# Optimization experiments

Measured on AMD Instinct MI355X. Metric: run time of the kernel, lower is better.

Reference implementation:

```python
import jax, jax.numpy as jnp
import numpy as np

EPS = 1e-5

def _ln(x, g, b):
    mu = jnp.mean(x, axis=-1, keepdims=True)
    var = jnp.mean(jnp.square(x - mu), axis=-1, keepdims=True)
    return (x - mu) * jax.lax.rsqrt(var + EPS) * g + b

def _gelu_new(x):
    # GPT-2 'gelu_new' (tanh approximation)
    c = jnp.asarray(np.sqrt(2.0 / np.pi), x.dtype)
    return 0.5 * x * (1.0 + jnp.tanh(c * (x + 0.044715 * x * x * x)))

def setup_inputs() -> dict:
    key = jax.random.key(0)
    ks = jax.random.split(key, 8)
    B, H, NH, HD, S = 16, 2048, 16, 128, 4096
    inv = lambda n: 1.0 / np.sqrt(n)
    return {
        "hidden_states": jax.random.normal(ks[0], (B, 1, H), jnp.float32),
        "cached_k": jax.random.normal(ks[1], (B, NH, S, HD), jnp.float32),
        "cached_v": jax.random.normal(ks[2], (B, NH, S, HD), jnp.float32),
        "ln1_g": jnp.ones((H,), jnp.float32),
        "ln1_b": jnp.zeros((H,), jnp.float32),
        "W_qkv": jax.random.normal(ks[3], (H, 3 * H), jnp.float32) * inv(H),
        "b_qkv": jnp.zeros((3 * H,), jnp.float32),
        "W_proj": jax.random.normal(ks[4], (H, H), jnp.float32) * inv(H),
        "b_proj": jnp.zeros((H,), jnp.float32),
        "ln2_g": jnp.ones((H,), jnp.float32),
        "ln2_b": jnp.zeros((H,), jnp.float32),
        "W_fc": jax.random.normal(ks[5], (H, 4 * H), jnp.float32) * inv(H),
        "b_fc": jnp.zeros((4 * H,), jnp.float32),
        "W_out": jax.random.normal(ks[6], (4 * H, H), jnp.float32) * inv(4 * H),
        "b_out": jnp.zeros((H,), jnp.float32),
    }

def reference(hidden_states, cached_k, cached_v, ln1_g, ln1_b, W_qkv, b_qkv,
              W_proj, b_proj, ln2_g, ln2_b, W_fc, b_fc, W_out, b_out):
    B, T, H = hidden_states.shape  # T == 1 (decode step)
    NH, HD = cached_k.shape[1], cached_k.shape[3]
    residual = hidden_states
    x = _ln(hidden_states, ln1_g, ln1_b)
    qkv = x @ W_qkv + b_qkv                        # [B,1,3H]
    q, k, v = jnp.split(qkv, 3, axis=-1)
    split = lambda t: t.reshape(B, T, NH, HD).transpose(0, 2, 1, 3)  # [B,NH,T,HD]
    q, k, v = split(q), split(k), split(v)
    k_full = jnp.concatenate([cached_k, k], axis=2)  # [B,NH,S+1,HD]
    v_full = jnp.concatenate([cached_v, v], axis=2)
    scale = 1.0 / jnp.sqrt(jnp.asarray(HD, q.dtype))
    scores = jnp.einsum('bhqd,bhkd->bhqk', q, k_full) * scale
    probs = jax.nn.softmax(scores, axis=-1)
    attn = jnp.einsum('bhqk,bhkd->bhqd', probs, v_full)  # [B,NH,1,HD]
    attn = attn.transpose(0, 2, 1, 3).reshape(B, T, H)
    attn = attn @ W_proj + b_proj
    h = attn + residual
    residual = h
    y = _ln(h, ln2_g, ln2_b)
    y = _gelu_new(y @ W_fc + b_fc) @ W_out + b_out
    return residual + y
```

## Files before the change

kernel.cpp:

```cpp
#include <hip/hip_runtime.h>
#include <hip/hip_bf16.h>

typedef unsigned int uint;


__global__ __launch_bounds__(256) void ln_f32_kernel(const float* __restrict__ in,
    const float* __restrict__ g, const float* __restrict__ bb, float* __restrict__ out)
{
    int row = blockIdx.x, t = threadIdx.x;
    const float* rp = in + row*2048;
    float4 a = ((const float4*)rp)[2*t];
    float4 b = ((const float4*)rp)[2*t+1];
    float v[8] = {a.x,a.y,a.z,a.w,b.x,b.y,b.z,b.w};
    float s=0.f, s2=0.f;
    #pragma unroll
    for(int i=0;i<8;i++){ s+=v[i]; s2+=v[i]*v[i]; }
    #pragma unroll
    for(int o=32;o>0;o>>=1){ s += __shfl_xor(s,o); s2 += __shfl_xor(s2,o); }
    __shared__ float red[8];
    int wv=t>>6, ln=t&63;
    if(ln==0){ red[wv]=s; red[4+wv]=s2; }
    __syncthreads();
    s  = red[0]+red[1]+red[2]+red[3];
    s2 = red[4]+red[5]+red[6]+red[7];
    float mu = s*(1.f/2048.f);
    float var = s2*(1.f/2048.f) - mu*mu;
    float rs = rsqrtf(var + 1e-5f);
    float4 g0 = ((const float4*)g)[2*t],  g1 = ((const float4*)g)[2*t+1];
    float4 b0 = ((const float4*)bb)[2*t], b1 = ((const float4*)bb)[2*t+1];
    float* op = out + row*2048 + t*8;
    float4 o0 = make_float4((v[0]-mu)*rs*g0.x+b0.x, (v[1]-mu)*rs*g0.y+b0.y,
                            (v[2]-mu)*rs*g0.z+b0.z, (v[3]-mu)*rs*g0.w+b0.w);
    float4 o1 = make_float4((v[4]-mu)*rs*g1.x+b1.x, (v[5]-mu)*rs*g1.y+b1.y,
                            (v[6]-mu)*rs*g1.z+b1.z, (v[7]-mu)*rs*g1.w+b1.w);
    ((float4*)op)[0]=o0; ((float4*)op)[1]=o1;
}

template<int KCHUNK>
__global__ __launch_bounds__(256) void gemm_sk(const float* __restrict__ X,
    const float* __restrict__ W, float* __restrict__ part, int K, int N, int colchunks)
{
    __shared__ float XS[16][KCHUNK];
    int cc = blockIdx.x % colchunks;
    int kc = blockIdx.x / colchunks;
    int k0 = kc * KCHUNK;
    for (int idx = threadIdx.x; idx < 16*KCHUNK; idx += 256){
        int m = idx / KCHUNK, i = idx % KCHUNK;
        XS[m][i] = X[m*K + k0 + i];
    }
    __syncthreads();
    int n0 = cc*512 + threadIdx.x*2;
    float a0[16], a1[16];
    #pragma unroll
    for(int m=0;m<16;m++){ a0[m]=0.f; a1[m]=0.f; }
    const float* Wp = W + (size_t)k0*N + n0;
    for (int i=0;i<KCHUNK;i+=4){
        float2 w0 = *(const float2*)(Wp + (size_t)(i+0)*N);
        float2 w1 = *(const float2*)(Wp + (size_t)(i+1)*N);
        float2 w2 = *(const float2*)(Wp + (size_t)(i+2)*N);
        float2 w3 = *(const float2*)(Wp + (size_t)(i+3)*N);
        #pragma unroll
        for(int m=0;m<16;m++){
            float4 x4 = *(const float4*)&XS[m][i];
            a0[m] += x4.x*w0.x + x4.y*w1.x + x4.z*w2.x + x4.w*w3.x;
            a1[m] += x4.x*w0.y + x4.y*w1.y + x4.z*w2.y + x4.w*w3.y;
        }
    }
    #pragma unroll
    for(int m=0;m<16;m++){
        *(float2*)&part[((size_t)(kc*16+m))*N + n0] = make_float2(a0[m], a1[m]);
    }
}

__global__ __launch_bounds__(256) void reduce_sk(const float* __restrict__ part, int N, int splitk,
    const float* __restrict__ bias, const float* __restrict__ res,
    float* __restrict__ outf, int mode)
{
    int n = blockIdx.x*256 + threadIdx.x;
    int m = blockIdx.y;
    size_t stride = (size_t)16*N;
    const float* p = part + (size_t)m*N + n;
    float s = 0.f;
    for (int kc=0;kc<splitk;kc++) s += p[(size_t)kc*stride];
    s += bias[n];
    if (mode==1 || mode==3) s += res[m*N+n];
    if (mode==2){
        float x = s;
        float t = tanhf(0.7978845608028654f*(x + 0.044715f*x*x*x));
        s = 0.5f*x*(1.f+t);
    }
    outf[m*N+n] = s;
}

__global__ __launch_bounds__(256) void attn_chunk(const float* __restrict__ qkv,
    const float* __restrict__ Kc, const float* __restrict__ Vc, float* __restrict__ part)
{
    int h = blockIdx.y, b = blockIdx.z;
    int wave = threadIdx.x >> 6, lane = threadIdx.x & 63;
    int wc = blockIdx.x*4 + wave;
    int jstart = wc * 128;
    const float* qrow = qkv + b*6144 + h*128;
    float2 q = *(const float2*)(qrow + 2*lane);
    size_t bh = (size_t)(b*16+h);
    const float* kp = Kc + bh*4096*128 + (size_t)jstart*128 + 2*lane;
    const float* vp = Vc + bh*4096*128 + (size_t)jstart*128 + 2*lane;
    float m = -1e30f, l = 0.f, o0 = 0.f, o1 = 0.f;
    #pragma unroll 4
    for (int j=0;j<128;++j){
        float2 kw = *(const float2*)kp;
        float2 vw = *(const float2*)vp;
        kp += 128; vp += 128;
        float p = q.x*kw.x + q.y*kw.y;
        p += __shfl_xor(p,32); p += __shfl_xor(p,16); p += __shfl_xor(p,8);
        p += __shfl_xor(p,4);  p += __shfl_xor(p,2);  p += __shfl_xor(p,1);
        float sc = p * 0.08838834764831845f;
        float mn = fmaxf(m, sc);
        float f  = __expf(m - mn);
        float e  = __expf(sc - mn);
        l  = l*f + e;
        o0 = o0*f + e*vw.x;
        o1 = o1*f + e*vw.y;
        m = mn;
    }
    if (wc == 31){
        const float* kn = qkv + b*6144 + 2048 + h*128;
        const float* vn = qkv + b*6144 + 4096 + h*128;
        float p = q.x*kn[2*lane] + q.y*kn[2*lane+1];
        p += __shfl_xor(p,32); p += __shfl_xor(p,16); p += __shfl_xor(p,8);
        p += __shfl_xor(p,4);  p += __shfl_xor(p,2);  p += __shfl_xor(p,1);
        float sc = p * 0.08838834764831845f;
        float mn = fmaxf(m, sc);
        float f  = __expf(m - mn);
        float e  = __expf(sc - mn);
        l  = l*f + e;
        o0 = o0*f + e*vn[2*lane];
        o1 = o1*f + e*vn[2*lane+1];
        m = mn;
    }
    float* pp = part + ((size_t)(b*16+h)*32 + wc)*132;
    if (lane==0){ pp[0]=m; pp[1]=l; }
    *(float2*)&pp[2+2*lane] = make_float2(o0,o1);
}

__global__ __launch_bounds__(64) void attn_combine(const float* __restrict__ part,
                                                   float* __restrict__ attn_out)
{
    int bh = blockIdx.x;
    int lane = threadIdx.x;
    const float* pp = part + (size_t)bh*32*132;
    float M = -1e30f;
    for (int kc=0;kc<32;kc++) M = fmaxf(M, pp[kc*132]);
    float den=0.f, a0=0.f, a1=0.f;
    for (int kc=0;kc<32;kc++){
        float f = __expf(pp[kc*132] - M);
        den += f * pp[kc*132+1];
        float2 o = *(const float2*)&pp[kc*132 + 2 + 2*lane];
        a0 += f*o.x; a1 += f*o.y;
    }
    float inv = 1.f/den;
    int b = bh>>4, h = bh&15;
    float* op = attn_out + b*2048 + h*128 + 2*lane;
    op[0]=a0*inv; op[1]=a1*inv;
}

extern "C" void kernel_launch(void* const* d_in, const int* in_sizes, int n_in,
                              void* d_out, int out_size, void* d_ws, size_t ws_size,
                              hipStream_t stream)
{
    const float* hid  = (const float*)d_in[0];
    const float* Kc   = (const float*)d_in[1];
    const float* Vc   = (const float*)d_in[2];
    const float* ln1g = (const float*)d_in[3];
    const float* ln1b = (const float*)d_in[4];
    const float* Wqkv = (const float*)d_in[5];
    const float* bqkv = (const float*)d_in[6];
    const float* Wproj= (const float*)d_in[7];
    const float* bproj= (const float*)d_in[8];
    const float* ln2g = (const float*)d_in[9];
    const float* ln2b = (const float*)d_in[10];
    const float* Wfc  = (const float*)d_in[11];
    const float* bfc  = (const float*)d_in[12];
    const float* Wout = (const float*)d_in[13];
    const float* bout = (const float*)d_in[14];

    float* ws      = (float*)d_ws;
    float* xln     = ws;
    float* qkv     = xln + 32768;
    float* attn_o  = qkv + 98304;
    float* hbuf    = attn_o + 32768;
    float* yln     = hbuf + 32768;
    float* act     = yln + 32768;
    float* apart   = act + 131072;
    float* gpart   = apart + 1081344;

    ln_f32_kernel<<<16,256,0,stream>>>(hid, ln1g, ln1b, xln);
    gemm_sk<64><<<12*32,256,0,stream>>>(xln, Wqkv, gpart, 2048, 6144, 12);
    reduce_sk<<<dim3(24,16),256,0,stream>>>(gpart, 6144, 32, bqkv, nullptr, qkv, 0);
    attn_chunk<<<dim3(8,16,16),256,0,stream>>>(qkv, Kc, Vc, apart);
    attn_combine<<<256,64,0,stream>>>(apart, attn_o);
    gemm_sk<64><<<4*32,256,0,stream>>>(attn_o, Wproj, gpart, 2048, 2048, 4);
    reduce_sk<<<dim3(8,16),256,0,stream>>>(gpart, 2048, 32, bproj, hid, hbuf, 1);
    ln_f32_kernel<<<16,256,0,stream>>>(hbuf, ln2g, ln2b, yln);
    gemm_sk<64><<<16*32,256,0,stream>>>(yln, Wfc, gpart, 2048, 8192, 16);
    reduce_sk<<<dim3(32,16),256,0,stream>>>(gpart, 8192, 32, bfc, nullptr, act, 2);
    gemm_sk<128><<<4*64,256,0,stream>>>(act, Wout, gpart, 8192, 2048, 4);
    reduce_sk<<<dim3(8,16),256,0,stream>>>(gpart, 2048, 64, bout, hbuf, (float*)d_out, 3);
    (void)in_sizes; (void)n_in; (void)out_size; (void)ws_size;
}
```

Before: 395.6 us.

## Restructure decode attention to process four keys per wave with 16-lane groups

Each wave now splits into four 16-lane groups, and each group handles a different key row with 8 contiguous floats per lane loaded as float4. This cuts the dot-product shuffle reduction from six steps to four and processes four keys per iteration instead of one. A shared running max is kept across groups so the partial sums can be added together at the end. The partial buffer stride is padded to 136 for aligned float4 stores, and the launch bounds gain an occupancy hint of 8 blocks per CU. The trade is extra cross-group shuffles per iteration and more registers for the eight-element accumulators.

```diff
diff --git a/kernel.cpp b/kernel.cpp
--- a/kernel.cpp
+++ b/kernel.cpp
@@ -92,54 +92,77 @@
     outf[m*N+n] = s;
 }
 
-__global__ __launch_bounds__(256) void attn_chunk(const float* __restrict__ qkv,
+__global__ __launch_bounds__(256, 8) void attn_chunk(const float* __restrict__ qkv,
     const float* __restrict__ Kc, const float* __restrict__ Vc, float* __restrict__ part)
 {
     int h = blockIdx.y, b = blockIdx.z;
     int wave = threadIdx.x >> 6, lane = threadIdx.x & 63;
     int wc = blockIdx.x*4 + wave;
+    int grp = lane >> 4, cl = lane & 15;
+    const float* qrow = qkv + b*6144 + h*128 + cl*8;
+    float4 qa = *(const float4*)qrow;
+    float4 qb = *(const float4*)(qrow + 4);
+    size_t bh = (size_t)(b*16+h);
+    const float* Kbase = Kc + bh*4096*128;
+    const float* Vbase = Vc + bh*4096*128;
     int jstart = wc * 128;
-    const float* qrow = qkv + b*6144 + h*128;
-    float2 q = *(const float2*)(qrow + 2*lane);
-    size_t bh = (size_t)(b*16+h);
-    const float* kp = Kc + bh*4096*128 + (size_t)jstart*128 + 2*lane;
-    const float* vp = Vc + bh*4096*128 + (size_t)jstart*128 + 2*lane;
-    float m = -1e30f, l = 0.f, o0 = 0.f, o1 = 0.f;
-    #pragma unroll 4
-    for (int j=0;j<128;++j){
-        float2 kw = *(const float2*)kp;
-        float2 vw = *(const float2*)vp;
-        kp += 128; vp += 128;
-        float p = q.x*kw.x + q.y*kw.y;
-        p += __shfl_xor(p,32); p += __shfl_xor(p,16); p += __shfl_xor(p,8);
-        p += __shfl_xor(p,4);  p += __shfl_xor(p,2);  p += __shfl_xor(p,1);
+    float m = -1e30f, l = 0.f;
+    float o[8];
+    #pragma unroll
+    for(int i=0;i<8;i++) o[i]=0.f;
+    #pragma unroll 2
+    for (int it=0; it<32; ++it){
+        size_t off = (size_t)(jstart + it*4 + grp)*128 + cl*8;
+        float4 ka = *(const float4*)(Kbase + off);
+        float4 kb = *(const float4*)(Kbase + off + 4);
+        float4 va = *(const float4*)(Vbase + off);
+        float4 vb = *(const float4*)(Vbase + off + 4);
+        float p = qa.x*ka.x + qa.y*ka.y + qa.z*ka.z + qa.w*ka.w
+                + qb.x*kb.x + qb.y*kb.y + qb.z*kb.z + qb.w*kb.w;
+        p += __shfl_xor(p,1); p += __shfl_xor(p,2);
+        p += __shfl_xor(p,4); p += __shfl_xor(p,8);
+        float sc = p * 0.08838834764831845f;
+        float t = fmaxf(sc, __shfl_xor(sc,16));
+        t = fmaxf(t, __shfl_xor(t,32));
+        float mn = fmaxf(m, t);
+        float f = __expf(m - mn);
+        float e = __expf(sc - mn);
+        l = l*f + e;
+        o[0]=o[0]*f + e*va.x; o[1]=o[1]*f + e*va.y;
+        o[2]=o[2]*f + e*va.z; o[3]=o[3]*f + e*va.w;
+        o[4]=o[4]*f + e*vb.x; o[5]=o[5]*f + e*vb.y;
+        o[6]=o[6]*f + e*vb.z; o[7]=o[7]*f + e*vb.w;
+        m = mn;
+    }
+    if (wc == 31){
+        const float* kn = qkv + b*6144 + 2048 + h*128 + cl*8;
+        const float* vn = qkv + b*6144 + 4096 + h*128 + cl*8;
+        float4 ka = *(const float4*)kn, kb = *(const float4*)(kn+4);
+        float4 va = *(const float4*)vn, vb = *(const float4*)(vn+4);
+        float p = qa.x*ka.x + qa.y*ka.y + qa.z*ka.z + qa.w*ka.w
+                + qb.x*kb.x + qb.y*kb.y + qb.z*kb.z + qb.w*kb.w;
+        p += __shfl_xor(p,1); p += __shfl_xor(p,2);
+        p += __shfl_xor(p,4); p += __shfl_xor(p,8);
         float sc = p * 0.08838834764831845f;
         float mn = fmaxf(m, sc);
-        float f  = __expf(m - mn);
-        float e  = __expf(sc - mn);
-        l  = l*f + e;
-        o0 = o0*f + e*vw.x;
-        o1 = o1*f + e*vw.y;
+        float f = __expf(m - mn);
+        float e = (grp==0) ? __expf(sc - mn) : 0.f;
+        l = l*f + e;
+        o[0]=o[0]*f + e*va.x; o[1]=o[1]*f + e*va.y;
+        o[2]=o[2]*f + e*va.z; o[3]=o[3]*f + e*va.w;
+        o[4]=o[4]*f + e*vb.x; o[5]=o[5]*f + e*vb.y;
+        o[6]=o[6]*f + e*vb.z; o[7]=o[7]*f + e*vb.w;
         m = mn;
     }
-    if (wc == 31){
-        const float* kn = qkv + b*6144 + 2048 + h*128;
-        const float* vn = qkv + b*6144 + 4096 + h*128;
-        float p = q.x*kn[2*lane] + q.y*kn[2*lane+1];
-        p += __shfl_xor(p,32); p += __shfl_xor(p,16); p += __shfl_xor(p,8);
-        p += __shfl_xor(p,4);  p += __shfl_xor(p,2);  p += __shfl_xor(p,1);
-        float sc = p * 0.08838834764831845f;
-        float mn = fmaxf(m, sc);
-        float f  = __expf(m - mn);
-        float e  = __expf(sc - mn);
-        l  = l*f + e;
-        o0 = o0*f + e*vn[2*lane];
-        o1 = o1*f + e*vn[2*lane+1];
-        m = mn;
-    }
-    float* pp = part + ((size_t)(b*16+h)*32 + wc)*132;
+    l += __shfl_xor(l,16); l += __shfl_xor(l,32);
+    #pragma unroll
+    for(int i=0;i<8;i++){ o[i] += __shfl_xor(o[i],16); o[i] += __shfl_xor(o[i],32); }
+    float* pp = part + ((size_t)bh*32 + wc)*136;
     if (lane==0){ pp[0]=m; pp[1]=l; }
-    *(float2*)&pp[2+2*lane] = make_float2(o0,o1);
+    if (lane<16){
+        *(float4*)&pp[4 + lane*8]     = make_float4(o[0],o[1],o[2],o[3]);
+        *(float4*)&pp[4 + lane*8 + 4] = make_float4(o[4],o[5],o[6],o[7]);
+    }
 }
 
 __global__ __launch_bounds__(64) void attn_combine(const float* __restrict__ part,
@@ -147,14 +170,14 @@
 {
     int bh = blockIdx.x;
     int lane = threadIdx.x;
-    const float* pp = part + (size_t)bh*32*132;
+    const float* pp = part + (size_t)bh*32*136;
     float M = -1e30f;
-    for (int kc=0;kc<32;kc++) M = fmaxf(M, pp[kc*132]);
+    for (int kc=0;kc<32;kc++) M = fmaxf(M, pp[kc*136]);
     float den=0.f, a0=0.f, a1=0.f;
     for (int kc=0;kc<32;kc++){
-        float f = __expf(pp[kc*132] - M);
-        den += f * pp[kc*132+1];
-        float2 o = *(const float2*)&pp[kc*132 + 2 + 2*lane];
+        float f = __expf(pp[kc*136] - M);
+        den += f * pp[kc*136+1];
+        float2 o = *(const float2*)&pp[kc*136 + 4 + 2*lane];
         a0 += f*o.x; a1 += f*o.y;
     }
     float inv = 1.f/den;
@@ -191,7 +214,7 @@
     float* yln     = hbuf + 32768;
     float* act     = yln + 32768;
     float* apart   = act + 131072;
-    float* gpart   = apart + 1081344;
+    float* gpart   = apart + 1114112;
 
     ln_f32_kernel<<<16,256,0,stream>>>(hid, ln1g, ln1b, xln);
     gemm_sk<64><<<12*32,256,0,stream>>>(xln, Wqkv, gpart, 2048, 6144, 12);
```

After: 399.8 us. Within noise of the previous version (+1.1%).
